# Kernel optimization log

Hardware: AMD Instinct MI355X
Metric: run time of the kernel (lower is better)

## Reference

```python
import jax, jax.numpy as jnp
import numpy as np

B, T, N, D = 8, 64, 196, 768
K, P = 8, 2
BOUND = 2.5
EPS = 1e-6


def _dct2_basis(T, P, dtype=jnp.float32):
    t = jnp.arange(T, dtype=dtype) + 0.5
    rows = [jnp.ones(T, dtype=dtype)]
    for p in range(1, P + 1):
        rows.append(jnp.cos(jnp.pi * p * t / T))
    Bm = jnp.stack(rows, axis=0)  # [P+1, T]
    return Bm / (jnp.sqrt(jnp.sum(Bm * Bm, axis=1, keepdims=True)) + EPS)


def setup_inputs() -> dict:
    key = jax.random.key(0)
    k1, k2, k3 = jax.random.split(key, 3)
    x = jax.random.normal(k1, (B, T, N, D), dtype=jnp.float32)
    valid_mask = jnp.ones((B, T, N), dtype=jnp.float32)
    # proj weight [K, D]; module orthonormalizes (QR of W.T) every forward,
    # so we materialize the already-orthonormalized parameter value here.
    W0 = jax.random.uniform(k2, (K, D), dtype=jnp.float32, minval=-0.05, maxval=0.05)
    Q, _ = jnp.linalg.qr(W0.T)          # [D, K] orthonormal cols
    proj_W = Q.T                         # [K, D]
    feat_in = K * (P + 3)                # K*(P+1+2) = 40
    bound = float(np.sqrt(6.0 / (feat_in + D)))
    W_raw = jax.random.uniform(k3, (feat_in, D), dtype=jnp.float32, minval=-bound, maxval=bound)
    beta = jnp.full((D,), 0.5, dtype=jnp.float32)
    return {"x": x, "valid_mask": valid_mask, "proj_W": proj_W, "W_raw": W_raw, "beta": beta}


def reference(x, valid_mask, proj_W, W_raw, beta):
    b, t, n, d = x.shape
    U = proj_W.T                                         # [D, K]
    v = jnp.einsum('btnd,dk->btnk', x, U)
    v = v * valid_mask[..., None]
    v_bnkt = jnp.transpose(v, (0, 2, 3, 1))              # [B, N, K, T]
    rms = jnp.sqrt(jnp.mean(v_bnkt * v_bnkt, axis=-1, keepdims=True) + EPS)
    v_bounded = BOUND * jnp.tanh(v_bnkt / (rms + EPS))
    Bmat = _dct2_basis(t, P, x.dtype)                    # [P+1, T]
    coeff = jnp.einsum('bnkt,pt->bnkp', v_bounded, Bmat)
    mean_feat = jnp.mean(v_bounded, axis=-1, keepdims=True)
    rms_feat = jnp.sqrt(jnp.mean(v_bounded * v_bounded, axis=-1, keepdims=True) + EPS)
    feats = jnp.concatenate([coeff, mean_feat, rms_feat], axis=-1).reshape(b, n, -1)  # [B,N,K*(P+3)]
    W = jax.nn.softplus(W_raw)                           # [feat_in, D]
    y = feats @ W                                        # [B, N, D]
    beta_s = jax.nn.sigmoid(beta)[None, None, None, :]
    h = x + beta_s * y[:, None, :, :]
    m = valid_mask[..., None]
    h = m * h + (1.0 - m) * x
    return (h, W)
```

## Files before the change

kernel.cpp:

```cpp
#include <hip/hip_runtime.h>
#include <math.h>

#define B_ 8
#define T_ 64
#define N_ 196
#define D_ 768
#define K_ 8
#define FEAT 40
#define EPSF 1e-6f

constexpr int ROWS = B_ * T_ * N_;
constexpr long long HSIZE = (long long)ROWS * D_;
constexpr int QPR = D_ / 4;
constexpr unsigned RSTRIDE = (unsigned)N_ * QPR;

typedef float v4f __attribute__((ext_vector_type(4)));

__device__ __forceinline__ float wredux(float v) {
#pragma unroll
    for (int off = 32; off > 0; off >>= 1)
        v += __shfl_xor(v, off, 64);
    return v;
}

__device__ __forceinline__ float dot4(v4f a, v4f b) {
    return a.x * b.x + a.y * b.y + a.z * b.z + a.w * b.w;
}

__global__ __launch_bounds__(256) void k_wsp(const float* __restrict__ wraw,
                                             const float* __restrict__ beta,
                                             float* __restrict__ wout,
                                             float* __restrict__ beta_s) {
    int i = blockIdx.x * blockDim.x + threadIdx.x;
    if (i < FEAT * D_) {
        float xw = wraw[i];
        wout[i] = fmaxf(xw, 0.0f) + log1pf(expf(-fabsf(xw)));
    }
    if (i < D_) beta_s[i] = 1.0f / (1.0f + expf(-beta[i]));
}

__global__ __launch_bounds__(256)
void k_fused(const float* __restrict__ x,
             const float* __restrict__ mask,
             const float* __restrict__ pw,
             const float* __restrict__ wsp,
             const float* __restrict__ beta_s,
             float* __restrict__ h) {
    __shared__ float vpart[T_][K_ + 1];
    __shared__ float sf[FEAT];
    __shared__ float ylds[D_];
    __shared__ float smask[T_];

    const int tid  = threadIdx.x;
    const int lane = tid & 63;
    const int w    = tid >> 6;
    const int bn   = blockIdx.x;
    const int b    = bn / N_;
    const int n    = bn - b * N_;

    v4f u[2][3];
#pragma unroll
    for (int kk = 0; kk < 2; kk++)
#pragma unroll
        for (int c = 0; c < 3; c++)
            u[kk][c] = *(const v4f*)(pw + (2 * w + kk) * D_ + c * 256 + lane * 4);

    if (tid < T_) smask[tid] = mask[(b * T_ + tid) * N_ + n];

    const v4f* x4 = (const v4f*)x;
    const unsigned rowq0 = (unsigned)((b * T_) * N_ + n) * QPR;
    unsigned qn = rowq0;
    v4f n0 = x4[qn + lane];
    v4f n1 = x4[qn + 64 + lane];
    v4f n2 = x4[qn + 128 + lane];
#pragma unroll 1
    for (int t = 0; t < T_; t++) {
        v4f c0 = n0, c1 = n1, c2 = n2;
        if (t < T_ - 1) {
            qn += RSTRIDE;
            n0 = x4[qn + lane];
            n1 = x4[qn + 64 + lane];
            n2 = x4[qn + 128 + lane];
        }
        float a0 = dot4(c0, u[0][0]) + dot4(c1, u[0][1]) + dot4(c2, u[0][2]);
        float a1 = dot4(c0, u[1][0]) + dot4(c1, u[1][1]) + dot4(c2, u[1][2]);
        a0 += __shfl_xor(a0, 1, 64);
        a1 += __shfl_xor(a1, 1, 64);
        float val = (lane & 1) ? a1 : a0;
        val += __shfl_xor(val, 2, 64);
        val += __shfl_xor(val, 4, 64);
        val += __shfl_xor(val, 8, 64);
        val += __shfl_xor(val, 16, 64);
        val += __shfl_xor(val, 32, 64);
        if (lane < 2) vpart[t][2 * w + lane] = val;
        if ((t & 7) == 7) __syncthreads();
    }
    __syncthreads();

#pragma unroll
    for (int kk = 0; kk < 2; kk++) {
        const int k = w + kk * 4;
        float v = vpart[lane][k] * smask[lane];
        float s2  = wredux(v * v);
        float rms = sqrtf(s2 * (1.0f / T_) + EPSF);
        float vb  = 2.5f * tanhf(v / (rms + EPSF));
        const float PI = 3.14159265358979323846f;
        float ph = PI * ((float)lane + 0.5f) / (float)T_;
        float c1 = cosf(ph), c2 = cosf(2.0f * ph);
        float n1 = wredux(c1 * c1), n2 = wredux(c2 * c2);
        float S1 = wredux(vb), Sc1 = wredux(vb * c1);
        float Sc2 = wredux(vb * c2), Sq = wredux(vb * vb);
        if (lane == 0) {
            float* o = sf + k * 5;
            o[0] = S1 / (8.0f + EPSF);
            o[1] = Sc1 / (sqrtf(n1) + EPSF);
            o[2] = Sc2 / (sqrtf(n2) + EPSF);
            o[3] = S1 * (1.0f / T_);
            o[4] = sqrtf(Sq * (1.0f / T_) + EPSF);
        }
    }
    __syncthreads();

    for (int d = tid; d < D_; d += 256) {
        float a0 = 0.f, a1 = 0.f;
#pragma unroll
        for (int f = 0; f < FEAT; f += 2) {
            a0 += sf[f]     * wsp[f * D_ + d];
            a1 += sf[f + 1] * wsp[(f + 1) * D_ + d];
        }
        ylds[d] = (a0 + a1) * beta_s[d];
    }
    __syncthreads();

    const v4f* y4 = (const v4f*)ylds;
    const v4f y0 = y4[lane], y1 = y4[64 + lane], y2 = y4[128 + lane];
    v4f* h4 = (v4f*)h;
    unsigned qD = (unsigned)((b * T_ + w * 16) * N_ + n) * QPR;
    v4f d0 = __builtin_nontemporal_load(x4 + qD + lane);
    v4f d1 = __builtin_nontemporal_load(x4 + qD + 64 + lane);
    v4f d2 = __builtin_nontemporal_load(x4 + qD + 128 + lane);
#pragma unroll 1
    for (int j = 0; j < 16; j++) {
        v4f c0 = d0, c1 = d1, c2 = d2;
        const unsigned qc = qD;
        if (j < 15) {
            qD += RSTRIDE;
            d0 = __builtin_nontemporal_load(x4 + qD + lane);
            d1 = __builtin_nontemporal_load(x4 + qD + 64 + lane);
            d2 = __builtin_nontemporal_load(x4 + qD + 128 + lane);
        }
        const float m = smask[w * 16 + j];
        __builtin_nontemporal_store(c0 + m * y0, h4 + qc + lane);
        __builtin_nontemporal_store(c1 + m * y1, h4 + qc + 64 + lane);
        __builtin_nontemporal_store(c2 + m * y2, h4 + qc + 128 + lane);
    }
}

extern "C" void kernel_launch(void* const* d_in, const int* in_sizes, int n_in,
                              void* d_out, int out_size, void* d_ws, size_t ws_size,
                              hipStream_t stream) {
    const float* x    = (const float*)d_in[0];
    const float* mask = (const float*)d_in[1];
    const float* pw   = (const float*)d_in[2];
    const float* wraw = (const float*)d_in[3];
    const float* beta = (const float*)d_in[4];

    float* h    = (float*)d_out;
    float* wout = h + HSIZE;
    float* beta_s = (float*)d_ws;

    hipLaunchKernelGGL(k_wsp, dim3((FEAT * D_ + 255) / 256), dim3(256), 0, stream,
                       wraw, beta, wout, beta_s);
    hipLaunchKernelGGL(k_fused, dim3(B_ * N_), dim3(256), 0, stream,
                       x, mask, pw, wout, beta_s, h);
}
```

Baseline: 174.9 us.

## Fuse softplus/sigmoid prep into main kernel, deepen x prefetch in output pass

Drops the separate weight-prep kernel launch. The main kernel now computes softplus of W_raw and sigmoid of beta inline when forming y, and one extra block writes the softplus W output. It also removes the periodic __syncthreads in the projection loop and changes the output pass to prefetch two timesteps ahead using ordinary loads instead of nontemporal loads. The trade is redundant transcendental work in every block (40x768 softplus per block) in exchange for one fewer launch and deeper memory pipelining.

```diff
diff --git a/kernel.cpp b/kernel.cpp
--- a/kernel.cpp
+++ b/kernel.cpp
@@ -9,6 +9,7 @@
 #define FEAT 40
 #define EPSF 1e-6f
 
+constexpr int BN = B_ * N_;
 constexpr int ROWS = B_ * T_ * N_;
 constexpr long long HSIZE = (long long)ROWS * D_;
 constexpr int QPR = D_ / 4;
@@ -27,34 +28,34 @@
     return a.x * b.x + a.y * b.y + a.z * b.z + a.w * b.w;
 }
 
-__global__ __launch_bounds__(256) void k_wsp(const float* __restrict__ wraw,
-                                             const float* __restrict__ beta,
-                                             float* __restrict__ wout,
-                                             float* __restrict__ beta_s) {
-    int i = blockIdx.x * blockDim.x + threadIdx.x;
-    if (i < FEAT * D_) {
-        float xw = wraw[i];
-        wout[i] = fmaxf(xw, 0.0f) + log1pf(expf(-fabsf(xw)));
-    }
-    if (i < D_) beta_s[i] = 1.0f / (1.0f + expf(-beta[i]));
+__device__ __forceinline__ float softplusf(float xw) {
+    return fmaxf(xw, 0.0f) + log1pf(expf(-fabsf(xw)));
 }
 
 __global__ __launch_bounds__(256)
 void k_fused(const float* __restrict__ x,
              const float* __restrict__ mask,
              const float* __restrict__ pw,
-             const float* __restrict__ wsp,
-             const float* __restrict__ beta_s,
-             float* __restrict__ h) {
+             const float* __restrict__ wraw,
+             const float* __restrict__ beta,
+             float* __restrict__ h,
+             float* __restrict__ wout) {
+    const int tid  = threadIdx.x;
+    const int bn   = blockIdx.x;
+
+    if (bn == BN) {
+        for (int i = tid; i < FEAT * D_; i += 256)
+            wout[i] = softplusf(wraw[i]);
+        return;
+    }
+
     __shared__ float vpart[T_][K_ + 1];
     __shared__ float sf[FEAT];
     __shared__ float ylds[D_];
     __shared__ float smask[T_];
 
-    const int tid  = threadIdx.x;
     const int lane = tid & 63;
     const int w    = tid >> 6;
-    const int bn   = blockIdx.x;
     const int b    = bn / N_;
     const int n    = bn - b * N_;
 
@@ -68,8 +69,7 @@
     if (tid < T_) smask[tid] = mask[(b * T_ + tid) * N_ + n];
 
     const v4f* x4 = (const v4f*)x;
-    const unsigned rowq0 = (unsigned)((b * T_) * N_ + n) * QPR;
-    unsigned qn = rowq0;
+    unsigned qn = (unsigned)((b * T_) * N_ + n) * QPR;
     v4f n0 = x4[qn + lane];
     v4f n1 = x4[qn + 64 + lane];
     v4f n2 = x4[qn + 128 + lane];
@@ -93,7 +93,6 @@
         val += __shfl_xor(val, 16, 64);
         val += __shfl_xor(val, 32, 64);
         if (lane < 2) vpart[t][2 * w + lane] = val;
-        if ((t & 7) == 7) __syncthreads();
     }
     __syncthreads();
 
@@ -125,34 +124,50 @@
         float a0 = 0.f, a1 = 0.f;
 #pragma unroll
         for (int f = 0; f < FEAT; f += 2) {
-            a0 += sf[f]     * wsp[f * D_ + d];
-            a1 += sf[f + 1] * wsp[(f + 1) * D_ + d];
+            a0 += sf[f]     * softplusf(wraw[f * D_ + d]);
+            a1 += sf[f + 1] * softplusf(wraw[(f + 1) * D_ + d]);
         }
-        ylds[d] = (a0 + a1) * beta_s[d];
+        float bs = 1.0f / (1.0f + expf(-beta[d]));
+        ylds[d] = (a0 + a1) * bs;
     }
     __syncthreads();
 
     const v4f* y4 = (const v4f*)ylds;
     const v4f y0 = y4[lane], y1 = y4[64 + lane], y2 = y4[128 + lane];
     v4f* h4 = (v4f*)h;
-    unsigned qD = (unsigned)((b * T_ + w * 16) * N_ + n) * QPR;
-    v4f d0 = __builtin_nontemporal_load(x4 + qD + lane);
-    v4f d1 = __builtin_nontemporal_load(x4 + qD + 64 + lane);
-    v4f d2 = __builtin_nontemporal_load(x4 + qD + 128 + lane);
+    const unsigned qD0 = (unsigned)((b * T_ + w * 16) * N_ + n) * QPR;
+    v4f Xa0 = x4[qD0 + lane];
+    v4f Xa1 = x4[qD0 + 64 + lane];
+    v4f Xa2 = x4[qD0 + 128 + lane];
+    v4f Xb0 = x4[qD0 + RSTRIDE + lane];
+    v4f Xb1 = x4[qD0 + RSTRIDE + 64 + lane];
+    v4f Xb2 = x4[qD0 + RSTRIDE + 128 + lane];
 #pragma unroll 1
-    for (int j = 0; j < 16; j++) {
-        v4f c0 = d0, c1 = d1, c2 = d2;
-        const unsigned qc = qD;
-        if (j < 15) {
-            qD += RSTRIDE;
-            d0 = __builtin_nontemporal_load(x4 + qD + lane);
-            d1 = __builtin_nontemporal_load(x4 + qD + 64 + lane);
-            d2 = __builtin_nontemporal_load(x4 + qD + 128 + lane);
+    for (int j = 0; j < 16; j += 2) {
+        const unsigned qa = qD0 + (unsigned)j * RSTRIDE;
+        const unsigned qb = qa + RSTRIDE;
+        const float ma = smask[w * 16 + j];
+        const float mb = smask[w * 16 + j + 1];
+        v4f h0 = Xa0 + ma * y0, h1 = Xa1 + ma * y1, h2 = Xa2 + ma * y2;
+        if (j + 2 < 16) {
+            const unsigned qn2 = qa + 2 * RSTRIDE;
+            Xa0 = x4[qn2 + lane];
+            Xa1 = x4[qn2 + 64 + lane];
+            Xa2 = x4[qn2 + 128 + lane];
         }
-        const float m = smask[w * 16 + j];
-        __builtin_nontemporal_store(c0 + m * y0, h4 + qc + lane);
-        __builtin_nontemporal_store(c1 + m * y1, h4 + qc + 64 + lane);
-        __builtin_nontemporal_store(c2 + m * y2, h4 + qc + 128 + lane);
+        __builtin_nontemporal_store(h0, h4 + qa + lane);
+        __builtin_nontemporal_store(h1, h4 + qa + 64 + lane);
+        __builtin_nontemporal_store(h2, h4 + qa + 128 + lane);
+        v4f g0 = Xb0 + mb * y0, g1 = Xb1 + mb * y1, g2 = Xb2 + mb * y2;
+        if (j + 3 < 16) {
+            const unsigned qn3 = qb + 2 * RSTRIDE;
+            Xb0 = x4[qn3 + lane];
+            Xb1 = x4[qn3 + 64 + lane];
+            Xb2 = x4[qn3 + 128 + lane];
+        }
+        __builtin_nontemporal_store(g0, h4 + qb + lane);
+        __builtin_nontemporal_store(g1, h4 + qb + 64 + lane);
+        __builtin_nontemporal_store(g2, h4 + qb + 128 + lane);
     }
 }
 
@@ -167,10 +182,7 @@
 
     float* h    = (float*)d_out;
     float* wout = h + HSIZE;
-    float* beta_s = (float*)d_ws;
 
-    hipLaunchKernelGGL(k_wsp, dim3((FEAT * D_ + 255) / 256), dim3(256), 0, stream,
-                       wraw, beta, wout, beta_s);
-    hipLaunchKernelGGL(k_fused, dim3(B_ * N_), dim3(256), 0, stream,
-                       x, mask, pw, wout, beta_s, h);
+    hipLaunchKernelGGL(k_fused, dim3(BN + 1), dim3(256), 0, stream,
+                       x, mask, pw, wraw, beta, h, wout);
 }
```

After: 323.7 us. +85.1%, slower.

## Stage x rows in double-buffered LDS so each wave loads distinct timesteps

Applied to the files above, without the earlier changes.

Before, every wave loaded the same full row of x at every timestep (4x redundant global/L2 reads) to compute its two projection outputs. Now each wave loads one distinct timestep row per tile into a double-buffered shared-memory buffer, and all waves read the four rows back from LDS. This cuts redundant global loads by 4x. In exchange it adds 24KB of LDS, LDS read traffic, and a block barrier per tile.

```diff
diff --git a/kernel.cpp b/kernel.cpp
--- a/kernel.cpp
+++ b/kernel.cpp
@@ -9,6 +9,7 @@
 #define FEAT 40
 #define EPSF 1e-6f
 
+constexpr int BN = B_ * N_;
 constexpr int ROWS = B_ * T_ * N_;
 constexpr long long HSIZE = (long long)ROWS * D_;
 constexpr int QPR = D_ / 4;
@@ -46,6 +47,7 @@
              const float* __restrict__ wsp,
              const float* __restrict__ beta_s,
              float* __restrict__ h) {
+    __shared__ v4f   xbuf[2][4][QPR];
     __shared__ float vpart[T_][K_ + 1];
     __shared__ float sf[FEAT];
     __shared__ float ylds[D_];
@@ -68,34 +70,47 @@
     if (tid < T_) smask[tid] = mask[(b * T_ + tid) * N_ + n];
 
     const v4f* x4 = (const v4f*)x;
-    const unsigned rowq0 = (unsigned)((b * T_) * N_ + n) * QPR;
-    unsigned qn = rowq0;
-    v4f n0 = x4[qn + lane];
-    v4f n1 = x4[qn + 64 + lane];
-    v4f n2 = x4[qn + 128 + lane];
+    const unsigned TSTRIDE = 4 * RSTRIDE;
+    unsigned q = (unsigned)((b * T_ + w) * N_ + n) * QPR;
+    v4f R0 = x4[q + lane], R1 = x4[q + 64 + lane], R2 = x4[q + 128 + lane];
+    xbuf[0][w][lane]       = R0;
+    xbuf[0][w][64 + lane]  = R1;
+    xbuf[0][w][128 + lane] = R2;
+    __syncthreads();
+    int p = 0;
 #pragma unroll 1
-    for (int t = 0; t < T_; t++) {
-        v4f c0 = n0, c1 = n1, c2 = n2;
-        if (t < T_ - 1) {
-            qn += RSTRIDE;
-            n0 = x4[qn + lane];
-            n1 = x4[qn + 64 + lane];
-            n2 = x4[qn + 128 + lane];
+    for (int tile = 0; tile < 16; ++tile) {
+        if (tile < 15) {
+            q += TSTRIDE;
+            R0 = x4[q + lane];
+            R1 = x4[q + 64 + lane];
+            R2 = x4[q + 128 + lane];
         }
-        float a0 = dot4(c0, u[0][0]) + dot4(c1, u[0][1]) + dot4(c2, u[0][2]);
-        float a1 = dot4(c0, u[1][0]) + dot4(c1, u[1][1]) + dot4(c2, u[1][2]);
-        a0 += __shfl_xor(a0, 1, 64);
-        a1 += __shfl_xor(a1, 1, 64);
-        float val = (lane & 1) ? a1 : a0;
-        val += __shfl_xor(val, 2, 64);
-        val += __shfl_xor(val, 4, 64);
-        val += __shfl_xor(val, 8, 64);
-        val += __shfl_xor(val, 16, 64);
-        val += __shfl_xor(val, 32, 64);
-        if (lane < 2) vpart[t][2 * w + lane] = val;
-        if ((t & 7) == 7) __syncthreads();
+#pragma unroll
+        for (int r = 0; r < 4; ++r) {
+            v4f c0 = xbuf[p][r][lane];
+            v4f c1 = xbuf[p][r][64 + lane];
+            v4f c2 = xbuf[p][r][128 + lane];
+            float a0 = dot4(c0, u[0][0]) + dot4(c1, u[0][1]) + dot4(c2, u[0][2]);
+            float a1 = dot4(c0, u[1][0]) + dot4(c1, u[1][1]) + dot4(c2, u[1][2]);
+            a0 += __shfl_xor(a0, 1, 64);
+            a1 += __shfl_xor(a1, 1, 64);
+            float val = (lane & 1) ? a1 : a0;
+            val += __shfl_xor(val, 2, 64);
+            val += __shfl_xor(val, 4, 64);
+            val += __shfl_xor(val, 8, 64);
+            val += __shfl_xor(val, 16, 64);
+            val += __shfl_xor(val, 32, 64);
+            if (lane < 2) vpart[tile * 4 + r][2 * w + lane] = val;
+        }
+        if (tile < 15) {
+            xbuf[p ^ 1][w][lane]       = R0;
+            xbuf[p ^ 1][w][64 + lane]  = R1;
+            xbuf[p ^ 1][w][128 + lane] = R2;
+        }
+        __syncthreads();
+        p ^= 1;
     }
-    __syncthreads();
 
 #pragma unroll
     for (int kk = 0; kk < 2; kk++) {
@@ -171,6 +186,6 @@
 
     hipLaunchKernelGGL(k_wsp, dim3((FEAT * D_ + 255) / 256), dim3(256), 0, stream,
                        wraw, beta, wout, beta_s);
-    hipLaunchKernelGGL(k_fused, dim3(B_ * N_), dim3(256), 0, stream,
+    hipLaunchKernelGGL(k_fused, dim3(BN), dim3(256), 0, stream,
                        x, mask, pw, wout, beta_s, h);
 }
```

Result: faster. 151.5 us (-13.4%).
